# Optimization experiments

Measured on AMD Instinct MI355X. Metric: run time of the kernel, lower is better.

Reference implementation:

```python
import jax, jax.numpy as jnp
import numpy as np

USER_SIZE = 1_000_000
ITEM_SIZE = 1_000_000
EMBED = 64
BATCH = 4096
NUM_TOTAL = 100
STD = 0.01


def setup_inputs() -> dict:
    key = jax.random.key(0)
    ks = jax.random.split(key, 16)
    d = {}
    d["user"] = jax.random.randint(ks[0], (BATCH, 1), 0, USER_SIZE, dtype=jnp.int64 if jax.config.jax_enable_x64 else jnp.int32)
    d["item"] = jax.random.randint(ks[1], (BATCH, NUM_TOTAL), 0, ITEM_SIZE, dtype=jnp.int64 if jax.config.jax_enable_x64 else jnp.int32)
    d["num_total"] = NUM_TOTAL
    # Embedding tables stored as [vocab, embed] (transpose of nn.Linear weight [embed, vocab])
    d["Wu_gmf"] = jax.random.normal(ks[2], (USER_SIZE, EMBED), jnp.float32) * STD
    d["bu_gmf"] = jnp.zeros((EMBED,), jnp.float32)
    d["Wu_mlp"] = jax.random.normal(ks[3], (USER_SIZE, EMBED), jnp.float32) * STD
    d["bu_mlp"] = jnp.zeros((EMBED,), jnp.float32)
    d["Wi_gmf"] = jax.random.normal(ks[4], (ITEM_SIZE, EMBED), jnp.float32) * STD
    d["bi_gmf"] = jnp.zeros((EMBED,), jnp.float32)
    d["Wi_mlp"] = jax.random.normal(ks[5], (ITEM_SIZE, EMBED), jnp.float32) * STD
    d["bi_mlp"] = jnp.zeros((EMBED,), jnp.float32)
    # MLP tower, stored as [in, out]
    d["W1"] = jax.random.normal(ks[6], (2 * EMBED, 2 * EMBED), jnp.float32) * STD
    d["b1"] = jnp.zeros((2 * EMBED,), jnp.float32)
    d["W2"] = jax.random.normal(ks[7], (2 * EMBED, EMBED), jnp.float32) * STD
    d["b2"] = jnp.zeros((EMBED,), jnp.float32)
    d["W3"] = jax.random.normal(ks[8], (EMBED, EMBED // 2), jnp.float32) * STD
    d["b3"] = jnp.zeros((EMBED // 2,), jnp.float32)
    d["Wp"] = jax.random.normal(ks[9], (3 * EMBED // 2, 1), jnp.float32) * STD
    d["bp"] = jnp.zeros((1,), jnp.float32)
    return d


def reference(user, item, num_total, Wu_gmf, bu_gmf, Wu_mlp, bu_mlp, Wi_gmf, bi_gmf, Wi_mlp, bi_mlp, W1, b1, W2, b2, W3, b3, Wp, bp):
    # one-hot @ Linear == embedding gather (column select of weight) + bias
    eu_g = Wu_gmf[user[:, 0]] + bu_gmf              # [B, E]
    eu_m = Wu_mlp[user[:, 0]] + bu_mlp              # [B, E]
    ei_g = Wi_gmf[item] + bi_gmf                    # [B, N, E]
    ei_m = Wi_mlp[item] + bi_mlp                    # [B, N, E]

    gmf = eu_g[:, None, :] * ei_g                   # [B, N, E]

    eu_m_b = jnp.broadcast_to(eu_m[:, None, :], ei_m.shape)
    inter = jnp.concatenate([eu_m_b, ei_m], axis=2)  # [B, N, 2E]
    h1 = jax.nn.relu(inter @ W1 + b1)
    h2 = jax.nn.relu(h1 @ W2 + b2)
    h3 = jax.nn.relu(h2 @ W3 + b3)                  # [B, N, E/2]

    concat = jnp.concatenate([gmf, h3], axis=2)     # [B, N, 3E/2]
    pred = jax.nn.sigmoid(concat @ Wp + bp)         # [B, N, 1]
    return pred[..., 0]                             # [B, N]
```

## Files before the change

kernel.cpp:

```cpp
#include <hip/hip_runtime.h>


typedef __attribute__((ext_vector_type(8))) short bf16x8;
typedef __attribute__((ext_vector_type(4))) float f32x4;

__device__ __forceinline__ short f2bf(float x){
  unsigned u = __float_as_uint(x);
  u += 0x7fffu + ((u >> 16) & 1u);
  return (short)(u >> 16);
}
__device__ __forceinline__ unsigned char f2fp8(float x){
  return (unsigned char)(__builtin_amdgcn_cvt_pk_fp8_f32(x, 0.f, 0, false) & 0xFF);
}


__global__ __launch_bounds__(256) void ncf_prep_w(
    const float* __restrict__ W1, const float* __restrict__ W2,
    const float* __restrict__ W3, const float* __restrict__ b1,
    const float* __restrict__ bi_mlp, char* __restrict__ ws)
{
  if (blockIdx.x == 104){
    int j = threadIdx.x;
    if (j < 128){
      float acc = b1[j];
      #pragma unroll 4
      for (int k = 0; k < 64; k++)
        acc += bi_mlp[k] * W1[(64 + k)*128 + j];
      ((float*)(ws + 34816))[j] = acc;
    }
    return;
  }
  int i = blockIdx.x * 256 + threadIdx.x;
  if (i < 8192){
    int col = i >> 6, k = i & 63;
    ((short*)ws)[i] = f2bf(W1[k*128 + col]);
  } else if (i < 16384){
    int t = i - 8192; int col = t >> 6, k = t & 63;
    ((unsigned char*)(ws + 16384))[t] = f2fp8(W1[(64 + k)*128 + col]);
  } else if (i < 24576){
    int t = i - 16384; int col = t >> 7, k = t & 127;
    ((unsigned char*)(ws + 24576))[t] = f2fp8(W2[k*64 + col]);
  } else {
    int t = i - 24576; int col = t >> 6, k = t & 63;
    ((unsigned char*)(ws + 32768))[t] = f2fp8(W3[k*32 + col]);
  }
}

__global__ __launch_bounds__(256) void ncf_prep_u(
    const int* __restrict__ user,
    const float* __restrict__ Wu_gmf, const float* __restrict__ bu_gmf,
    const float* __restrict__ Wu_mlp, const float* __restrict__ bu_mlp,
    const float* __restrict__ bi_gmf, const float* __restrict__ Wp,
    const short* __restrict__ W1uT, const float* __restrict__ c1,
    float* __restrict__ Xu, float* __restrict__ wup, float* __restrict__ cu)
{
  __shared__ __align__(16) short s_eu[64][72];
  const int tid = threadIdx.x;
  const int r = tid >> 2, q = tid & 3;
  const int b = blockIdx.x * 64 + r;
  long u = (long)user[b];
  {
    const float4* ump = (const float4*)(Wu_mlp + u*64) + q*4;
    const float4* bmp = (const float4*)(bu_mlp) + q*4;
    const float4* ugp = (const float4*)(Wu_gmf + u*64) + q*4;
    const float4* bgp = (const float4*)(bu_gmf) + q*4;
    const float4* wpp = (const float4*)(Wp) + q*4;
    const float4* bip = (const float4*)(bi_gmf) + q*4;
    float4* wdst = (float4*)(wup + (long)b*64) + q*4;
    bf16x8 ea[2];
    float cacc = 0.f;
    #pragma unroll
    for (int j = 0; j < 4; j++){
      float4 m = ump[j], mb = bmp[j];
      int h = j >> 1, s = (j & 1) * 4;
      ea[h][s+0] = f2bf(m.x + mb.x); ea[h][s+1] = f2bf(m.y + mb.y);
      ea[h][s+2] = f2bf(m.z + mb.z); ea[h][s+3] = f2bf(m.w + mb.w);
      float4 g = ugp[j], gb = bgp[j], wp = wpp[j], bi = bip[j];
      float4 wg; wg.x = (g.x+gb.x)*wp.x; wg.y = (g.y+gb.y)*wp.y;
                 wg.z = (g.z+gb.z)*wp.z; wg.w = (g.w+gb.w)*wp.w;
      wdst[j] = wg;
      cacc += wg.x*bi.x + wg.y*bi.y + wg.z*bi.z + wg.w*bi.w;
    }
    *(bf16x8*)&s_eu[r][q*16]     = ea[0];
    *(bf16x8*)&s_eu[r][q*16 + 8] = ea[1];
    cacc += __shfl_xor(cacc, 1);
    cacc += __shfl_xor(cacc, 2);
    if (q == 0) cu[b] = cacc;
  }
  __syncthreads();

  const int w = tid >> 6, l = tid & 63, lr = l & 15, lg = l >> 4;
  f32x4 acc[4][2];
  #pragma unroll
  for (int mt = 0; mt < 4; mt++)
    #pragma unroll
    for (int nt = 0; nt < 2; nt++)
      acc[mt][nt] = (f32x4){0.f, 0.f, 0.f, 0.f};
  #pragma unroll
  for (int ks = 0; ks < 2; ks++){
    bf16x8 af[4];
    #pragma unroll
    for (int mt = 0; mt < 4; mt++)
      af[mt] = *(const bf16x8*)&s_eu[mt*16 + lr][ks*32 + lg*8];
    #pragma unroll
    for (int nt = 0; nt < 2; nt++){
      bf16x8 bf_ = *(const bf16x8*)&W1uT[(w*32 + nt*16 + lr)*64 + ks*32 + lg*8];
      #pragma unroll
      for (int mt = 0; mt < 4; mt++)
        acc[mt][nt] = __builtin_amdgcn_mfma_f32_16x16x32_bf16(af[mt], bf_, acc[mt][nt], 0, 0, 0);
    }
  }
  #pragma unroll
  for (int nt = 0; nt < 2; nt++){
    int col = w*32 + nt*16 + lr;
    float cc = c1[col];
    #pragma unroll
    for (int mt = 0; mt < 4; mt++)
      #pragma unroll
      for (int rr = 0; rr < 4; rr++){
        int row = mt*16 + lg*4 + rr;
        Xu[(long)(blockIdx.x*64 + row)*128 + col] = acc[mt][nt][rr] + cc;
      }
  }
}

__global__ __launch_bounds__(256) void ncf_main(
    const int* __restrict__ item,
    const float* __restrict__ Wi_mlp, const float* __restrict__ Wi_gmf,
    const unsigned char* __restrict__ W1iT, const unsigned char* __restrict__ W2T,
    const unsigned char* __restrict__ W3T,
    const float* __restrict__ b2, const float* __restrict__ b3,
    const float* __restrict__ Wp, const float* __restrict__ bp,
    const float* __restrict__ Xu, const float* __restrict__ wup,
    const float* __restrict__ cu,
    float* __restrict__ out, int N, int total, int Bsz)
{
  __shared__ __align__(16) unsigned char s_item[64][80];
  __shared__ __align__(16) unsigned char s_h1[64][136];
  __shared__ __align__(16) unsigned char s_h2[64][80];
  __shared__ __align__(16) float s_xu[2][128];
  __shared__            float s_pg[64];

  const int tid = threadIdx.x;
  const int p0  = blockIdx.x * 64;
  const int b0  = p0 / N;
  const int thr = (b0 + 1) * N;
  const int r   = tid >> 2, q = tid & 3;
  const int w   = tid >> 6, l = tid & 63;
  const int lr  = l & 15,  lg = l >> 4;
  const float bp0 = bp[0];

  {
    int p = p0 + r;
    int b = b0 + ((p >= thr) ? 1 : 0);
    long ib = (long)item[p] * 64;
    const float4* mp = (const float4*)(Wi_mlp + ib) + q*4;
    const float4* gp = (const float4*)(Wi_gmf + ib) + q*4;
    const float4* wq = (const float4*)(wup + (long)b*64) + q*4;
    float pg = 0.f;
    int pk[4];
    #pragma unroll
    for (int j = 0; j < 4; j++){
      float4 m = mp[j], g = gp[j], wv = wq[j];
      pg += g.x*wv.x + g.y*wv.y + g.z*wv.z + g.w*wv.w;
      int t_ = __builtin_amdgcn_cvt_pk_fp8_f32(m.x, m.y, 0, false);
      t_     = __builtin_amdgcn_cvt_pk_fp8_f32(m.z, m.w, t_, true);
      pk[j] = t_;
    }
    *(int4*)&s_item[r][q*16] = (int4){pk[0], pk[1], pk[2], pk[3]};
    pg += __shfl_xor(pg, 1);
    pg += __shfl_xor(pg, 2);
    if (q == 0) s_pg[r] = pg + cu[b];
    int i2 = tid >> 7, col = tid & 127;
    int bb = b0 + i2; if (bb >= Bsz) bb = Bsz - 1;
    s_xu[i2][col] = Xu[(long)bb*128 + col];
  }
  __syncthreads();

  {
    f32x4 acc[2][4];
    #pragma unroll
    for (int mt = 0; mt < 2; mt++)
      #pragma unroll
      for (int nt = 0; nt < 4; nt++)
        acc[mt][nt] = (f32x4){0.f, 0.f, 0.f, 0.f};
    #pragma unroll
    for (int ks = 0; ks < 2; ks++){
      long bfrag[4];
      #pragma unroll
      for (int nt = 0; nt < 4; nt++)
        bfrag[nt] = *(const long*)&s_item[nt*16 + lr][ks*32 + lg*8];
      #pragma unroll
      for (int mt = 0; mt < 2; mt++){
        long af = *(const long*)&W1iT[((w*2 + mt)*16 + lr)*64 + ks*32 + lg*8];
        #pragma unroll
        for (int nt = 0; nt < 4; nt++)
          acc[mt][nt] = __builtin_amdgcn_mfma_f32_16x16x32_fp8_fp8(af, bfrag[nt], acc[mt][nt], 0, 0, 0);
      }
    }
    #pragma unroll
    for (int mt = 0; mt < 2; mt++){
      int colb = (w*2 + mt)*16 + lg*4;
      #pragma unroll
      for (int nt = 0; nt < 4; nt++){
        int pair = nt*16 + lr;
        int bl = (p0 + pair >= thr) ? 1 : 0;
        float4 xv = *(const float4*)&s_xu[bl][colb];
        float v0 = acc[mt][nt][0] + xv.x; v0 = v0 > 0.f ? v0 : 0.f;
        float v1 = acc[mt][nt][1] + xv.y; v1 = v1 > 0.f ? v1 : 0.f;
        float v2 = acc[mt][nt][2] + xv.z; v2 = v2 > 0.f ? v2 : 0.f;
        float v3 = acc[mt][nt][3] + xv.w; v3 = v3 > 0.f ? v3 : 0.f;
        int t_ = __builtin_amdgcn_cvt_pk_fp8_f32(v0, v1, 0, false);
        t_     = __builtin_amdgcn_cvt_pk_fp8_f32(v2, v3, t_, true);
        *(int*)&s_h1[pair][colb] = t_;
      }
    }
  }
  __syncthreads();

  {
    f32x4 acc[4];
    #pragma unroll
    for (int nt = 0; nt < 4; nt++) acc[nt] = (f32x4){0.f, 0.f, 0.f, 0.f};
    #pragma unroll
    for (int ks = 0; ks < 4; ks++){
      long af = *(const long*)&W2T[(w*16 + lr)*128 + ks*32 + lg*8];
      #pragma unroll
      for (int nt = 0; nt < 4; nt++){
        long bf_ = *(const long*)&s_h1[nt*16 + lr][ks*32 + lg*8];
        acc[nt] = __builtin_amdgcn_mfma_f32_16x16x32_fp8_fp8(af, bf_, acc[nt], 0, 0, 0);
      }
    }
    int colb = w*16 + lg*4;
    float4 b2v = *(const float4*)&b2[colb];
    #pragma unroll
    for (int nt = 0; nt < 4; nt++){
      int pair = nt*16 + lr;
      float v0 = acc[nt][0] + b2v.x; v0 = v0 > 0.f ? v0 : 0.f;
      float v1 = acc[nt][1] + b2v.y; v1 = v1 > 0.f ? v1 : 0.f;
      float v2 = acc[nt][2] + b2v.z; v2 = v2 > 0.f ? v2 : 0.f;
      float v3 = acc[nt][3] + b2v.w; v3 = v3 > 0.f ? v3 : 0.f;
      int t_ = __builtin_amdgcn_cvt_pk_fp8_f32(v0, v1, 0, false);
      t_     = __builtin_amdgcn_cvt_pk_fp8_f32(v2, v3, t_, true);
      *(int*)&s_h2[pair][colb] = t_;
    }
  }
  __syncthreads();

  {
    f32x4 acc[2];
    #pragma unroll
    for (int mt = 0; mt < 2; mt++) acc[mt] = (f32x4){0.f, 0.f, 0.f, 0.f};
    #pragma unroll
    for (int ks = 0; ks < 2; ks++){
      long bf_ = *(const long*)&s_h2[w*16 + lr][ks*32 + lg*8];
      #pragma unroll
      for (int mt = 0; mt < 2; mt++){
        long af = *(const long*)&W3T[(mt*16 + lr)*64 + ks*32 + lg*8];
        acc[mt] = __builtin_amdgcn_mfma_f32_16x16x32_fp8_fp8(af, bf_, acc[mt], 0, 0, 0);
      }
    }
    float t = 0.f;
    #pragma unroll
    for (int mt = 0; mt < 2; mt++){
      int colb = mt*16 + lg*4;
      float4 b3v = *(const float4*)&b3[colb];
      float4 wpv = *(const float4*)&Wp[64 + colb];
      float v0 = acc[mt][0] + b3v.x; v0 = v0 > 0.f ? v0 : 0.f;
      float v1 = acc[mt][1] + b3v.y; v1 = v1 > 0.f ? v1 : 0.f;
      float v2 = acc[mt][2] + b3v.z; v2 = v2 > 0.f ? v2 : 0.f;
      float v3 = acc[mt][3] + b3v.w; v3 = v3 > 0.f ? v3 : 0.f;
      t += v0*wpv.x + v1*wpv.y + v2*wpv.z + v3*wpv.w;
    }
    t += __shfl_xor(t, 16);
    t += __shfl_xor(t, 32);
    if (l < 16){
      int pair = w*16 + l;
      int p = p0 + pair;
      if (p < total){
        float z = t + s_pg[pair] + bp0;
        out[p] = 1.f / (1.f + __expf(-z));
      }
    }
  }
}

extern "C" void kernel_launch(void* const* d_in, const int* in_sizes, int n_in,
                              void* d_out, int out_size, void* d_ws, size_t ws_size,
                              hipStream_t stream)
{
  const int*   user   = (const int*)  d_in[0];
  const int*   item   = (const int*)  d_in[1];
  const float* Wu_gmf = (const float*)d_in[3];
  const float* bu_gmf = (const float*)d_in[4];
  const float* Wu_mlp = (const float*)d_in[5];
  const float* bu_mlp = (const float*)d_in[6];
  const float* Wi_gmf = (const float*)d_in[7];
  const float* bi_gmf = (const float*)d_in[8];
  const float* Wi_mlp = (const float*)d_in[9];
  const float* bi_mlp = (const float*)d_in[10];
  const float* W1     = (const float*)d_in[11];
  const float* b1     = (const float*)d_in[12];
  const float* W2     = (const float*)d_in[13];
  const float* b2     = (const float*)d_in[14];
  const float* W3     = (const float*)d_in[15];
  const float* b3     = (const float*)d_in[16];
  const float* Wp     = (const float*)d_in[17];
  const float* bp     = (const float*)d_in[18];

  int B     = in_sizes[0];
  int total = in_sizes[1];
  int N     = total / B;

  char* wsb = (char*)d_ws;
  short*         W1uT = (short*)wsb;
  unsigned char* W1iT = (unsigned char*)(wsb + 16384);
  unsigned char* W2T  = (unsigned char*)(wsb + 24576);
  unsigned char* W3T  = (unsigned char*)(wsb + 32768);
  float*         c1   = (float*)(wsb + 34816);
  float*         Xu   = (float*)(wsb + 36864);
  float*         wup  = Xu  + (size_t)B * 128;
  float*         cuv  = wup + (size_t)B * 64;

  ncf_prep_w<<<105, 256, 0, stream>>>(W1, W2, W3, b1, bi_mlp, wsb);
  ncf_prep_u<<<B/64, 256, 0, stream>>>(user, Wu_gmf, bu_gmf, Wu_mlp, bu_mlp,
                                       bi_gmf, Wp, W1uT, c1, Xu, wup, cuv);

  int nblk = (total + 63) / 64;
  ncf_main<<<nblk, 256, 0, stream>>>(item, Wi_mlp, Wi_gmf,
      W1iT, W2T, W3T, b2, b3, Wp, bp, Xu, wup, cuv,
      (float*)d_out, N, total, B);
}
```

Measured before the change: 71.69 us.

## Make each wave process an independent 16-pair tile without block barriers

Restructures the main kernel so every wave owns its own 16 item-pair tile end to end. Each wave loads its item embeddings straight into MFMA B fragments in registers and keeps per-wave LDS buffers. The block-wide __syncthreads are replaced with wave-local lgkmcnt waits. This removes cross-wave barrier stalls and the shared staging of item rows. In exchange, each wave now reloads the full W1/W2 weight fragments from global or cache, since output columns are no longer split across waves, and gathers are less coalesced per wave.

```diff
diff --git a/kernel.cpp b/kernel.cpp
--- a/kernel.cpp
+++ b/kernel.cpp
@@ -3,6 +3,8 @@
 
 typedef __attribute__((ext_vector_type(8))) short bf16x8;
 typedef __attribute__((ext_vector_type(4))) float f32x4;
+
+union i2l { int2 i; long v; };
 
 __device__ __forceinline__ short f2bf(float x){
   unsigned u = __float_as_uint(x);
@@ -11,6 +13,10 @@
 }
 __device__ __forceinline__ unsigned char f2fp8(float x){
   return (unsigned char)(__builtin_amdgcn_cvt_pk_fp8_f32(x, 0.f, 0, false) & 0xFF);
+}
+__device__ __forceinline__ void wave_lds_fence(){
+  asm volatile("s_waitcnt lgkmcnt(0)" ::: "memory");
+  __builtin_amdgcn_sched_barrier(0);
 }
 
 
@@ -133,127 +139,127 @@
     const float* __restrict__ Wp, const float* __restrict__ bp,
     const float* __restrict__ Xu, const float* __restrict__ wup,
     const float* __restrict__ cu,
-    float* __restrict__ out, int N, int total, int Bsz)
+    float* __restrict__ out, int N, int total, int nmt, int Bsz)
 {
-  __shared__ __align__(16) unsigned char s_item[64][80];
-  __shared__ __align__(16) unsigned char s_h1[64][136];
-  __shared__ __align__(16) unsigned char s_h2[64][80];
-  __shared__ __align__(16) float s_xu[2][128];
-  __shared__            float s_pg[64];
+  __shared__ __align__(16) unsigned char s_h1[4][16*136];
+  __shared__ __align__(16) unsigned char s_h2[4][16*72];
+  __shared__ __align__(16) float s_xu[4][256];
 
   const int tid = threadIdx.x;
-  const int p0  = blockIdx.x * 64;
+  const int w  = tid >> 6, l = tid & 63;
+  const int lr = l & 15,  lg = l >> 4;
+  unsigned char* h1 = &s_h1[w][0];
+  unsigned char* h2 = &s_h2[w][0];
+  float* xu = &s_xu[w][0];
+
+  const int mt0 = blockIdx.x*4 + w;
+  if (mt0 >= nmt) return;
+  const int p0  = mt0 * 16;
   const int b0  = p0 / N;
   const int thr = (b0 + 1) * N;
-  const int r   = tid >> 2, q = tid & 3;
-  const int w   = tid >> 6, l = tid & 63;
-  const int lr  = l & 15,  lg = l >> 4;
-  const float bp0 = bp[0];
-
-  {
-    int p = p0 + r;
-    int b = b0 + ((p >= thr) ? 1 : 0);
-    long ib = (long)item[p] * 64;
-    const float4* mp = (const float4*)(Wi_mlp + ib) + q*4;
-    const float4* gp = (const float4*)(Wi_gmf + ib) + q*4;
-    const float4* wq = (const float4*)(wup + (long)b*64) + q*4;
-    float pg = 0.f;
-    int pk[4];
+
+  int p = p0 + lr; if (p >= total) p = total - 1;
+  const int  bA = b0 + ((p >= thr) ? 1 : 0);
+  const long ib = (long)item[p] * 64;
+
+  long a1[2];
+  #pragma unroll
+  for (int ks = 0; ks < 2; ks++){
+    const float4* ap = (const float4*)(Wi_mlp + ib + ks*32 + lg*8);
+    float4 x = ap[0], y = ap[1];
+    int t0 = __builtin_amdgcn_cvt_pk_fp8_f32(x.x, x.y, 0, false);
+    t0     = __builtin_amdgcn_cvt_pk_fp8_f32(x.z, x.w, t0, true);
+    int t1 = __builtin_amdgcn_cvt_pk_fp8_f32(y.x, y.y, 0, false);
+    t1     = __builtin_amdgcn_cvt_pk_fp8_f32(y.z, y.w, t1, true);
+    i2l u; u.i.x = t0; u.i.y = t1;
+    a1[ks] = u.v;
+  }
+
+  float pg;
+  {
+    const float4* gp = (const float4*)(Wi_gmf + ib + lg*16);
+    const float4* wq = (const float4*)(wup + (long)bA*64 + lg*16);
+    float s = 0.f;
     #pragma unroll
     for (int j = 0; j < 4; j++){
-      float4 m = mp[j], g = gp[j], wv = wq[j];
-      pg += g.x*wv.x + g.y*wv.y + g.z*wv.z + g.w*wv.w;
-      int t_ = __builtin_amdgcn_cvt_pk_fp8_f32(m.x, m.y, 0, false);
-      t_     = __builtin_amdgcn_cvt_pk_fp8_f32(m.z, m.w, t_, true);
-      pk[j] = t_;
-    }
-    *(int4*)&s_item[r][q*16] = (int4){pk[0], pk[1], pk[2], pk[3]};
-    pg += __shfl_xor(pg, 1);
-    pg += __shfl_xor(pg, 2);
-    if (q == 0) s_pg[r] = pg + cu[b];
-    int i2 = tid >> 7, col = tid & 127;
-    int bb = b0 + i2; if (bb >= Bsz) bb = Bsz - 1;
-    s_xu[i2][col] = Xu[(long)bb*128 + col];
-  }
-  __syncthreads();
-
-  {
-    f32x4 acc[2][4];
-    #pragma unroll
-    for (int mt = 0; mt < 2; mt++)
-      #pragma unroll
-      for (int nt = 0; nt < 4; nt++)
-        acc[mt][nt] = (f32x4){0.f, 0.f, 0.f, 0.f};
-    #pragma unroll
-    for (int ks = 0; ks < 2; ks++){
-      long bfrag[4];
-      #pragma unroll
-      for (int nt = 0; nt < 4; nt++)
-        bfrag[nt] = *(const long*)&s_item[nt*16 + lr][ks*32 + lg*8];
-      #pragma unroll
-      for (int mt = 0; mt < 2; mt++){
-        long af = *(const long*)&W1iT[((w*2 + mt)*16 + lr)*64 + ks*32 + lg*8];
-        #pragma unroll
-        for (int nt = 0; nt < 4; nt++)
-          acc[mt][nt] = __builtin_amdgcn_mfma_f32_16x16x32_fp8_fp8(af, bfrag[nt], acc[mt][nt], 0, 0, 0);
+      float4 g = gp[j], v = wq[j];
+      s += g.x*v.x + g.y*v.y + g.z*v.z + g.w*v.w;
+    }
+    s += __shfl_xor(s, 16);
+    s += __shfl_xor(s, 32);
+    pg = s + cu[bA];
+  }
+
+  {
+    int row = l >> 5;
+    int col = (l & 31) * 4;
+    int bb = b0 + row; if (bb >= Bsz) bb = Bsz - 1;
+    *(float4*)&xu[row*128 + col] = *(const float4*)&Xu[(long)bb*128 + col];
+  }
+  wave_lds_fence();
+  const int bl = (p0 + lr >= thr) ? 1 : 0;
+
+  {
+    f32x4 acc[8];
+    #pragma unroll
+    for (int mt = 0; mt < 8; mt++) acc[mt] = (f32x4){0.f,0.f,0.f,0.f};
+    #pragma unroll
+    for (int ks = 0; ks < 2; ks++)
+      #pragma unroll
+      for (int mt = 0; mt < 8; mt++){
+        long af = *(const long*)&W1iT[(mt*16 + lr)*64 + ks*32 + lg*8];
+        acc[mt] = __builtin_amdgcn_mfma_f32_16x16x32_fp8_fp8(af, a1[ks], acc[mt], 0, 0, 0);
       }
-    }
-    #pragma unroll
-    for (int mt = 0; mt < 2; mt++){
-      int colb = (w*2 + mt)*16 + lg*4;
-      #pragma unroll
-      for (int nt = 0; nt < 4; nt++){
-        int pair = nt*16 + lr;
-        int bl = (p0 + pair >= thr) ? 1 : 0;
-        float4 xv = *(const float4*)&s_xu[bl][colb];
-        float v0 = acc[mt][nt][0] + xv.x; v0 = v0 > 0.f ? v0 : 0.f;
-        float v1 = acc[mt][nt][1] + xv.y; v1 = v1 > 0.f ? v1 : 0.f;
-        float v2 = acc[mt][nt][2] + xv.z; v2 = v2 > 0.f ? v2 : 0.f;
-        float v3 = acc[mt][nt][3] + xv.w; v3 = v3 > 0.f ? v3 : 0.f;
-        int t_ = __builtin_amdgcn_cvt_pk_fp8_f32(v0, v1, 0, false);
-        t_     = __builtin_amdgcn_cvt_pk_fp8_f32(v2, v3, t_, true);
-        *(int*)&s_h1[pair][colb] = t_;
-      }
-    }
-  }
-  __syncthreads();
-
-  {
-    f32x4 acc[4];
-    #pragma unroll
-    for (int nt = 0; nt < 4; nt++) acc[nt] = (f32x4){0.f, 0.f, 0.f, 0.f};
-    #pragma unroll
-    for (int ks = 0; ks < 4; ks++){
-      long af = *(const long*)&W2T[(w*16 + lr)*128 + ks*32 + lg*8];
-      #pragma unroll
-      for (int nt = 0; nt < 4; nt++){
-        long bf_ = *(const long*)&s_h1[nt*16 + lr][ks*32 + lg*8];
-        acc[nt] = __builtin_amdgcn_mfma_f32_16x16x32_fp8_fp8(af, bf_, acc[nt], 0, 0, 0);
-      }
-    }
-    int colb = w*16 + lg*4;
-    float4 b2v = *(const float4*)&b2[colb];
-    #pragma unroll
-    for (int nt = 0; nt < 4; nt++){
-      int pair = nt*16 + lr;
-      float v0 = acc[nt][0] + b2v.x; v0 = v0 > 0.f ? v0 : 0.f;
-      float v1 = acc[nt][1] + b2v.y; v1 = v1 > 0.f ? v1 : 0.f;
-      float v2 = acc[nt][2] + b2v.z; v2 = v2 > 0.f ? v2 : 0.f;
-      float v3 = acc[nt][3] + b2v.w; v3 = v3 > 0.f ? v3 : 0.f;
+    #pragma unroll
+    for (int mt = 0; mt < 8; mt++){
+      int colb = mt*16 + lg*4;
+      float4 xv = *(const float4*)&xu[bl*128 + colb];
+      float v0 = acc[mt][0] + xv.x; v0 = v0 > 0.f ? v0 : 0.f;
+      float v1 = acc[mt][1] + xv.y; v1 = v1 > 0.f ? v1 : 0.f;
+      float v2 = acc[mt][2] + xv.z; v2 = v2 > 0.f ? v2 : 0.f;
+      float v3 = acc[mt][3] + xv.w; v3 = v3 > 0.f ? v3 : 0.f;
       int t_ = __builtin_amdgcn_cvt_pk_fp8_f32(v0, v1, 0, false);
       t_     = __builtin_amdgcn_cvt_pk_fp8_f32(v2, v3, t_, true);
-      *(int*)&s_h2[pair][colb] = t_;
-    }
-  }
-  __syncthreads();
+      *(int*)&h1[lr*136 + colb] = t_;
+    }
+  }
+  wave_lds_fence();
+
+  {
+    f32x4 acc[4];
+    #pragma unroll
+    for (int mt = 0; mt < 4; mt++) acc[mt] = (f32x4){0.f,0.f,0.f,0.f};
+    #pragma unroll
+    for (int ks = 0; ks < 4; ks++){
+      long bf_ = *(const long*)&h1[lr*136 + ks*32 + lg*8];
+      #pragma unroll
+      for (int mt = 0; mt < 4; mt++){
+        long af = *(const long*)&W2T[(mt*16 + lr)*128 + ks*32 + lg*8];
+        acc[mt] = __builtin_amdgcn_mfma_f32_16x16x32_fp8_fp8(af, bf_, acc[mt], 0, 0, 0);
+      }
+    }
+    #pragma unroll
+    for (int mt = 0; mt < 4; mt++){
+      int colb = mt*16 + lg*4;
+      float4 b2v = *(const float4*)&b2[colb];
+      float v0 = acc[mt][0] + b2v.x; v0 = v0 > 0.f ? v0 : 0.f;
+      float v1 = acc[mt][1] + b2v.y; v1 = v1 > 0.f ? v1 : 0.f;
+      float v2 = acc[mt][2] + b2v.z; v2 = v2 > 0.f ? v2 : 0.f;
+      float v3 = acc[mt][3] + b2v.w; v3 = v3 > 0.f ? v3 : 0.f;
+      int t_ = __builtin_amdgcn_cvt_pk_fp8_f32(v0, v1, 0, false);
+      t_     = __builtin_amdgcn_cvt_pk_fp8_f32(v2, v3, t_, true);
+      *(int*)&h2[lr*72 + colb] = t_;
+    }
+  }
+  wave_lds_fence();
 
   {
     f32x4 acc[2];
     #pragma unroll
-    for (int mt = 0; mt < 2; mt++) acc[mt] = (f32x4){0.f, 0.f, 0.f, 0.f};
+    for (int mt = 0; mt < 2; mt++) acc[mt] = (f32x4){0.f,0.f,0.f,0.f};
     #pragma unroll
     for (int ks = 0; ks < 2; ks++){
-      long bf_ = *(const long*)&s_h2[w*16 + lr][ks*32 + lg*8];
+      long bf_ = *(const long*)&h2[lr*72 + ks*32 + lg*8];
       #pragma unroll
       for (int mt = 0; mt < 2; mt++){
         long af = *(const long*)&W3T[(mt*16 + lr)*64 + ks*32 + lg*8];
@@ -274,13 +280,9 @@
     }
     t += __shfl_xor(t, 16);
     t += __shfl_xor(t, 32);
-    if (l < 16){
-      int pair = w*16 + l;
-      int p = p0 + pair;
-      if (p < total){
-        float z = t + s_pg[pair] + bp0;
-        out[p] = 1.f / (1.f + __expf(-z));
-      }
+    if (l < 16 && p0 + lr < total){
+      float z = t + pg + bp[0];
+      out[p0 + lr] = 1.f / (1.f + __expf(-z));
     }
   }
 }
@@ -326,8 +328,9 @@
   ncf_prep_u<<<B/64, 256, 0, stream>>>(user, Wu_gmf, bu_gmf, Wu_mlp, bu_mlp,
                                        bi_gmf, Wp, W1uT, c1, Xu, wup, cuv);
 
-  int nblk = (total + 63) / 64;
+  int nmt  = (total + 15) / 16;
+  int nblk = (nmt + 3) / 4;
   ncf_main<<<nblk, 256, 0, stream>>>(item, Wi_mlp, Wi_gmf,
       W1iT, W2T, W3T, b2, b3, Wp, bp, Xu, wup, cuv,
-      (float*)d_out, N, total, B);
-}
+      (float*)d_out, N, total, nmt, B);
+}
```

Result: slower. 123.6 us (+72.4%).
